# Performance work log

Measured on AMD Instinct MI355X. Metric: run time of the kernel, lower is better.

The kernel has to match this reference:

```python
import jax, jax.numpy as jnp
import numpy as np
from jax import lax

NPOINT = 2048
NSAMPLE = 32
RADIUS = 0.2


def setup_inputs() -> dict:
    key = jax.random.key(0)
    ks = jax.random.split(key, 6)
    B, N, C = 4, 16384, 64
    xyz = jax.random.normal(ks[0], (B, N, 3), jnp.float32)
    features = jax.random.normal(ks[1], (B, C, N), jnp.float32)

    def w(k, o, i):
        return jax.random.normal(k, (o, i), jnp.float32) * (1.0 / np.sqrt(i))

    W1 = w(ks[2], 64, C + 3)
    b1 = jnp.zeros((64,), jnp.float32)
    W2 = w(ks[3], 64, 64)
    b2 = jnp.zeros((64,), jnp.float32)
    W3 = w(ks[4], 128, 64)
    b3 = jnp.zeros((128,), jnp.float32)
    return {"xyz": xyz, "features": features, "W1": W1, "b1": b1,
            "W2": W2, "b2": b2, "W3": W3, "b3": b3}


def _fps(xyz, npoint):
    # Iterative furthest point sampling. xyz: (B, N, 3) -> (B, npoint) int32.
    B, N, _ = xyz.shape

    def step(carry, _):
        dist, last = carry  # dist: (B, N) running min sq-dist to chosen set
        p = jnp.take_along_axis(xyz, last[:, None, None], axis=1)  # (B,1,3)
        d = jnp.sum((xyz - p) ** 2, axis=-1)                        # (B,N)
        dist = jnp.minimum(dist, d)
        nxt = jnp.argmax(dist, axis=-1).astype(jnp.int32)
        return (dist, nxt), nxt

    init = (jnp.full((B, N), 1e10, xyz.dtype), jnp.zeros((B,), jnp.int32))
    _, rest = lax.scan(step, init, None, length=npoint - 1)  # (npoint-1, B)
    idx = jnp.concatenate([jnp.zeros((1, B), jnp.int32), rest], axis=0)
    return idx.T  # (B, npoint)


def _ball_query(xyz, new_xyz):
    # For each centroid pick up to NSAMPLE points within RADIUS (first-found
    # semantics, matching the PointNet++ CUDA ball_query: pad with first hit).
    B, N, _ = xyz.shape
    d2 = jnp.sum((new_xyz[:, :, None, :] - xyz[:, None, :, :]) ** 2, axis=-1)  # (B,S,N)
    cand = jnp.where(d2 < RADIUS * RADIUS, jnp.arange(N, dtype=jnp.int32), N)
    neg_vals, _ = lax.top_k(-cand, NSAMPLE)  # smallest NSAMPLE indices, in order
    sel = -neg_vals                           # (B,S,NSAMPLE)
    first = sel[..., :1]
    sel = jnp.where(sel == N, first, sel)     # pad empties with first hit
    return jnp.where(sel == N, 0, sel)        # fully-empty balls -> index 0


def reference(xyz, features, W1, b1, W2, b2, W3, b3):
    new_xyz_idx = _fps(xyz, NPOINT)                              # (B, S)
    new_xyz = jnp.take_along_axis(xyz, new_xyz_idx[..., None], axis=1)  # (B,S,3)
    idx = _ball_query(xyz, new_xyz)                              # (B,S,ns)
    B, S, ns = idx.shape
    C = features.shape[1]
    # Gather + center neighbor xyz: (B, 3, S, ns)
    gx = jnp.take_along_axis(xyz, idx.reshape(B, S * ns, 1), axis=1)
    gx = gx.reshape(B, S, ns, 3) - new_xyz[:, :, None, :]
    gx = gx.transpose(0, 3, 1, 2)
    # Gather neighbor features: (B, C, S, ns)
    gf = jnp.take_along_axis(features, idx.reshape(B, 1, S * ns), axis=2)
    gf = gf.reshape(B, C, S, ns)
    x = jnp.concatenate([gx, gf], axis=1)  # (B, C+3, S, ns)
    # SharedMLP: 1x1 conv + ReLU stack
    for W, b in ((W1, b1), (W2, b2), (W3, b3)):
        x = jax.nn.relu(jnp.einsum('oi,bisn->bosn', W, x) + b[None, :, None, None])
    new_features = x.max(axis=-1)  # (B, 128, S)
    return new_xyz, new_xyz_idx, new_features, idx
```

## Files before the change

kernel.cpp:

```cpp
#include <hip/hip_runtime.h>
#include <cstdint>

#define BATCH   4
#define NPTS    16384
#define NCH     64
#define NPOINT  2048
#define NSAMP   32

#define OFF_XYZ  0
#define OFF_IDX1 (BATCH*NPOINT*3)
#define OFF_FEAT (OFF_IDX1 + BATCH*NPOINT)
#define OFF_IDX3 (OFF_FEAT + BATCH*128*NPOINT)


__device__ __forceinline__ float sqd_exact(float dx, float dy, float dz) {
    float a = __fmul_rn(dx, dx);
    float b = __fmul_rn(dy, dy);
    float c = __fmul_rn(dz, dz);
    return __fadd_rn(__fadd_rn(a, b), c);
}

__device__ __forceinline__ int part3(int v) {
    return (v & 1) | ((v & 2) << 2) | ((v & 4) << 4) | ((v & 8) << 6);
}

__global__ __launch_bounds__(1024)
void binsort_kernel(const float* __restrict__ xyz, float* __restrict__ out) {
    const int b = blockIdx.x, t = threadIdx.x, lane = t & 63, wv = t >> 6;
    float* scr  = out + OFF_FEAT;
    float* sx   = scr + (size_t)b * NPTS;
    float* sy   = scr + (size_t)(BATCH + b) * NPTS;
    float* sz   = scr + (size_t)(2 * BATCH + b) * NPTS;
    int*   sidx = (int*)(scr + (size_t)3 * BATCH * NPTS) + (size_t)b * NPTS;
    const float* xb = xyz + (size_t)b * (NPTS * 3);

    __shared__ int hist[4096];
    __shared__ int wsum[16];
    for (int k = t; k < 4096; k += 1024) hist[k] = 0;
    __syncthreads();

    const int base = t << 4;
    float f[48];
    {
        const float4* v4 = (const float4*)(xb + (size_t)base * 3);
#pragma unroll
        for (int q = 0; q < 12; ++q) {
            float4 v = v4[q];
            f[4*q+0] = v.x; f[4*q+1] = v.y; f[4*q+2] = v.z; f[4*q+3] = v.w;
        }
    }
    int cells[16];
    const float sc = 16.0f / 9.0f;
#pragma unroll
    for (int j = 0; j < 16; ++j) {
        int qx = (int)fminf(fmaxf((f[3*j+0] + 4.5f) * sc, 0.0f), 15.0f);
        int qy = (int)fminf(fmaxf((f[3*j+1] + 4.5f) * sc, 0.0f), 15.0f);
        int qz = (int)fminf(fmaxf((f[3*j+2] + 4.5f) * sc, 0.0f), 15.0f);
        cells[j] = part3(qx) | (part3(qy) << 1) | (part3(qz) << 2);
        atomicAdd(&hist[cells[j]], 1);
    }
    __syncthreads();

    int h0 = hist[4*t], h1 = hist[4*t+1], h2 = hist[4*t+2], h3 = hist[4*t+3];
    int s = h0 + h1 + h2 + h3;
    int ps = s;
#pragma unroll
    for (int off = 1; off <= 32; off <<= 1) {
        int o = __shfl_up(ps, off, 64);
        if (lane >= off) ps += o;
    }
    if (lane == 63) wsum[wv] = ps;
    __syncthreads();
    int wbase = 0;
    for (int w = 0; w < wv; ++w) wbase += wsum[w];
    int excl = wbase + ps - s;
    hist[4*t]   = excl;
    hist[4*t+1] = excl + h0;
    hist[4*t+2] = excl + h0 + h1;
    hist[4*t+3] = excl + h0 + h1 + h2;
    __syncthreads();

#pragma unroll
    for (int j = 0; j < 16; ++j) {
        int pos = atomicAdd(&hist[cells[j]], 1);
        sx[pos] = f[3*j+0]; sy[pos] = f[3*j+1]; sz[pos] = f[3*j+2];
        sidx[pos] = base + j;
    }
}

__global__ __launch_bounds__(1024, 4)
void fps_kernel(const float* __restrict__ xyz, float* __restrict__ out) {
    const int b = blockIdx.x, t = threadIdx.x, lane = t & 63, wv = t >> 6;
    const float* scr  = out + OFF_FEAT;
    const float* sxp  = scr + (size_t)b * NPTS;
    const float* syp  = scr + (size_t)(BATCH + b) * NPTS;
    const float* szp  = scr + (size_t)(2 * BATCH + b) * NPTS;
    const int*   sip  = (const int*)(scr + (size_t)3 * BATCH * NPTS) + (size_t)b * NPTS;
    const float* __restrict__ xb = xyz + (size_t)b * (NPTS * 3);
    float* oxyz = out + OFF_XYZ  + (size_t)b * (NPOINT * 3);
    float* oidx = out + OFF_IDX1 + (size_t)b * NPOINT;

    const int base = t << 4;
    float px[16], py[16], pz[16], dist[16];
    unsigned idx2[8];
    {
        const float4* vx = (const float4*)(sxp + base);
        const float4* vy = (const float4*)(syp + base);
        const float4* vz = (const float4*)(szp + base);
        const int4*   vi = (const int4*)(sip + base);
#pragma unroll
        for (int q = 0; q < 4; ++q) {
            float4 a = vx[q]; px[4*q] = a.x; px[4*q+1] = a.y; px[4*q+2] = a.z; px[4*q+3] = a.w;
            float4 c = vy[q]; py[4*q] = c.x; py[4*q+1] = c.y; py[4*q+2] = c.z; py[4*q+3] = c.w;
            float4 d = vz[q]; pz[4*q] = d.x; pz[4*q+1] = d.y; pz[4*q+2] = d.z; pz[4*q+3] = d.w;
            int4   i = vi[q];
            idx2[2*q]   = (unsigned)i.x | ((unsigned)i.y << 16);
            idx2[2*q+1] = (unsigned)i.z | ((unsigned)i.w << 16);
        }
    }
    float bnx = px[0], bxx = px[0], bny = py[0], bxy = py[0], bnz = pz[0], bxz = pz[0];
#pragma unroll
    for (int j = 1; j < 16; ++j) {
        bnx = fminf(bnx, px[j]); bxx = fmaxf(bxx, px[j]);
        bny = fminf(bny, py[j]); bxy = fmaxf(bxy, py[j]);
        bnz = fminf(bnz, pz[j]); bxz = fmaxf(bxz, pz[j]);
    }
#pragma unroll
    for (int j = 0; j < 16; ++j) dist[j] = 1e10f;
    unsigned long long mk = 0;
    float maxdG = 1e10f;

    __shared__ unsigned long long s_k[2][16];

    float cx = xb[0], cy = xb[1], cz = xb[2];
    if (t == 0) { oxyz[0] = cx; oxyz[1] = cy; oxyz[2] = cz; oidx[0] = 0.0f; }

    for (int it = 1; it < NPOINT; ++it) {
        const int q = it & 1;
        float dxl = fmaxf(fmaxf(bnx - cx, cx - bxx), 0.0f);
        float dyl = fmaxf(fmaxf(bny - cy, cy - bxy), 0.0f);
        float dzl = fmaxf(fmaxf(bnz - cz, cz - bxz), 0.0f);
        float bb  = dxl * dxl + dyl * dyl + dzl * dzl;
        if (bb * 0.99999f < maxdG) {
            float mv = 0.0f;
#pragma unroll
            for (int j = 0; j < 16; ++j) {
                float d  = sqd_exact(__fsub_rn(px[j], cx),
                                     __fsub_rn(py[j], cy),
                                     __fsub_rn(pz[j], cz));
                float nd = fminf(dist[j], d);
                dist[j] = nd;
                mv = fmaxf(mv, nd);
            }
            int bi = 0xFFFF;
#pragma unroll
            for (int j = 0; j < 16; ++j) {
                int oi = (int)((idx2[j >> 1] >> ((j & 1) * 16)) & 0xFFFFu);
                if (dist[j] == mv) bi = min(bi, oi);
            }
            mk = ((unsigned long long)__float_as_uint(mv) << 32) | (unsigned)(~bi);
            maxdG = mv;
        }
        unsigned long long k = mk;
#pragma unroll
        for (int off = 32; off >= 1; off >>= 1) {
            unsigned long long o = __shfl_xor(k, off, 64);
            if (o > k) k = o;
        }
        if (lane == 0) s_k[q][wv] = k;
        __syncthreads();
        unsigned long long gk = s_k[q][0];
#pragma unroll
        for (int w = 1; w < 16; ++w) {
            unsigned long long v = s_k[q][w];
            if (v > gk) gk = v;
        }
        const int gi = (int)(~(unsigned)gk);
        cx = xb[gi*3+0]; cy = xb[gi*3+1]; cz = xb[gi*3+2];
        if (t == 0) {
            oxyz[it*3+0] = cx; oxyz[it*3+1] = cy; oxyz[it*3+2] = cz;
            oidx[it] = (float)gi;
        }
    }
}

__global__ __launch_bounds__(256)
void ballq_kernel(const float* __restrict__ xyz, float* __restrict__ out) {
    const int b    = blockIdx.y;
    const int t    = threadIdx.x;
    const int lane = t & 63;
    const int wv   = t >> 6;
    const int s    = blockIdx.x * 4 + wv;
    const float* __restrict__ xb = xyz + (size_t)b * (NPTS * 3);

    const float* ctr = out + OFF_XYZ + ((size_t)(b * NPOINT + s)) * 3;
    const float cx = ctr[0], cy = ctr[1], cz = ctr[2];

    __shared__ float sx[256], sy[256], sz[256];
    __shared__ int   lists[4][NSAMP];

    int have = 0;
    for (int tile = 0; tile < NPTS / 256; ++tile) {
        const int pi = tile * 256 + t;
        const float* p = xb + (size_t)pi * 3;
        float ax = p[0], ay = p[1], az = p[2];
        sx[t] = ax; sy[t] = ay; sz[t] = az;
        __syncthreads();
        if (have < NSAMP) {
#pragma unroll
            for (int sub = 0; sub < 4; ++sub) {
                const int li = sub * 64 + lane;
                float d2 = sqd_exact(__fsub_rn(cx, sx[li]),
                                     __fsub_rn(cy, sy[li]),
                                     __fsub_rn(cz, sz[li]));
                bool hit = d2 < 0.04f;
                unsigned long long m = __ballot(hit);
                if (hit) {
                    int pos = have + (int)__popcll(m & ((1ull << lane) - 1ull));
                    if (pos < NSAMP) lists[wv][pos] = tile * 256 + li;
                }
                have += (int)__popcll(m);
                if (have >= NSAMP) break;
            }
        }
        __syncthreads();
    }
    if (lane < NSAMP) {
        int hv = have < NSAMP ? have : NSAMP;
        int v0 = (have > 0) ? lists[wv][0] : 0;
        int v  = (lane < hv) ? lists[wv][lane] : v0;
        out[OFF_IDX3 + ((size_t)(b * NPOINT + s)) * NSAMP + lane] = (float)v;
    }
}

__global__ __launch_bounds__(256)
void mlp_kernel(const float* __restrict__ xyz, const float* __restrict__ feat,
                const float* __restrict__ W1, const float* __restrict__ b1,
                const float* __restrict__ W2, const float* __restrict__ b2,
                const float* __restrict__ W3, const float* __restrict__ b3,
                float* __restrict__ out) {
    const int s = blockIdx.x;
    const int b = blockIdx.y;
    const int t = threadIdx.x;

    __shared__ __align__(16) float Wbuf[64 * 128];
    __shared__ float Xs[67 * 32];
    __shared__ float H1[64 * 32];
    __shared__ float H2[64 * 32];
    __shared__ int   idxs[NSAMP];
    __shared__ float ctr[3];

    if (t < NSAMP) idxs[t] = (int)out[OFF_IDX3 + ((size_t)(b * NPOINT + s)) * NSAMP + t];
    if (t < 3)     ctr[t]  = out[OFF_XYZ + ((size_t)(b * NPOINT + s)) * 3 + t];
    for (int k = t; k < 67 * 64; k += 256) {
        int i = k >> 6, o = k & 63;
        Wbuf[k] = W1[o * 67 + i];
    }
    __syncthreads();

    const float* xb = xyz  + (size_t)b * (NPTS * 3);
    const float* fb = feat + (size_t)b * (NCH * NPTS);
    for (int k = t; k < 67 * 32; k += 256) {
        int i = k >> 5, n = k & 31;
        int ii = idxs[n];
        float v;
        if (i < 3) v = __fsub_rn(xb[(size_t)ii * 3 + i], ctr[i]);
        else       v = fb[(size_t)(i - 3) * NPTS + ii];
        Xs[k] = v;
    }
    __syncthreads();

    const int n  = t & 31;
    const int og = t >> 5;

    {
        const int o0 = og * 8;
        float acc[8] = {0,0,0,0,0,0,0,0};
        for (int i = 0; i < 67; ++i) {
            float x = Xs[i * 32 + n];
            const float4* wp = (const float4*)&Wbuf[i * 64 + o0];
            float4 w0 = wp[0], w1 = wp[1];
            acc[0] += w0.x * x; acc[1] += w0.y * x; acc[2] += w0.z * x; acc[3] += w0.w * x;
            acc[4] += w1.x * x; acc[5] += w1.y * x; acc[6] += w1.z * x; acc[7] += w1.w * x;
        }
#pragma unroll
        for (int k = 0; k < 8; ++k)
            H1[(o0 + k) * 32 + n] = fmaxf(acc[k] + b1[o0 + k], 0.0f);
    }
    __syncthreads();
    for (int k = t; k < 64 * 64; k += 256) {
        int i = k >> 6, o = k & 63;
        Wbuf[k] = W2[o * 64 + i];
    }
    __syncthreads();

    {
        const int o0 = og * 8;
        float acc[8] = {0,0,0,0,0,0,0,0};
        for (int i = 0; i < 64; ++i) {
            float x = H1[i * 32 + n];
            const float4* wp = (const float4*)&Wbuf[i * 64 + o0];
            float4 w0 = wp[0], w1 = wp[1];
            acc[0] += w0.x * x; acc[1] += w0.y * x; acc[2] += w0.z * x; acc[3] += w0.w * x;
            acc[4] += w1.x * x; acc[5] += w1.y * x; acc[6] += w1.z * x; acc[7] += w1.w * x;
        }
#pragma unroll
        for (int k = 0; k < 8; ++k)
            H2[(o0 + k) * 32 + n] = fmaxf(acc[k] + b2[o0 + k], 0.0f);
    }
    __syncthreads();
    for (int k = t; k < 64 * 128; k += 256) {
        int i = k >> 7, o = k & 127;
        Wbuf[k] = W3[o * 64 + i];
    }
    __syncthreads();

    {
        const int o0 = og * 16;
        float acc[16];
#pragma unroll
        for (int k = 0; k < 16; ++k) acc[k] = 0.0f;
        for (int i = 0; i < 64; ++i) {
            float x = H2[i * 32 + n];
            const float4* wp = (const float4*)&Wbuf[i * 128 + o0];
            float4 w0 = wp[0], w1 = wp[1], w2 = wp[2], w3 = wp[3];
            acc[0]  += w0.x * x; acc[1]  += w0.y * x; acc[2]  += w0.z * x; acc[3]  += w0.w * x;
            acc[4]  += w1.x * x; acc[5]  += w1.y * x; acc[6]  += w1.z * x; acc[7]  += w1.w * x;
            acc[8]  += w2.x * x; acc[9]  += w2.y * x; acc[10] += w2.z * x; acc[11] += w2.w * x;
            acc[12] += w3.x * x; acc[13] += w3.y * x; acc[14] += w3.z * x; acc[15] += w3.w * x;
        }
#pragma unroll
        for (int k = 0; k < 16; ++k) {
            float h = fmaxf(acc[k] + b3[o0 + k], 0.0f);
#pragma unroll
            for (int off = 16; off >= 1; off >>= 1)
                h = fmaxf(h, __shfl_xor(h, off, 64));
            if (n == 0)
                out[OFF_FEAT + (size_t)b * 128 * NPOINT + (size_t)(o0 + k) * NPOINT + s] = h;
        }
    }
}

extern "C" void kernel_launch(void* const* d_in, const int* in_sizes, int n_in,
                              void* d_out, int out_size, void* d_ws, size_t ws_size,
                              hipStream_t stream) {
    const float* xyz  = (const float*)d_in[0];
    const float* feat = (const float*)d_in[1];
    const float* W1   = (const float*)d_in[2];
    const float* b1   = (const float*)d_in[3];
    const float* W2   = (const float*)d_in[4];
    const float* b2   = (const float*)d_in[5];
    const float* W3   = (const float*)d_in[6];
    const float* b3   = (const float*)d_in[7];
    float* out = (float*)d_out;

    binsort_kernel<<<BATCH, 1024, 0, stream>>>(xyz, out);
    fps_kernel<<<BATCH, 1024, 0, stream>>>(xyz, out);
    ballq_kernel<<<dim3(NPOINT / 4, BATCH), 256, 0, stream>>>(xyz, out);
    mlp_kernel<<<dim3(NPOINT, BATCH), 256, 0, stream>>>(xyz, feat, W1, b1, W2, b2, W3, b3, out);
}
```

Baseline: 3.336 ms.

## Restructure FPS argmax reduction to carry winner coordinates and avoid global reload

The FPS loop now tracks the argmax index and its coordinates inside each thread's update, replacing the packed 64-bit key with a float max shuffle plus ballot-based tie-breaking. The cross-wave reduction is done by 16 threads with shuffles, and the winner's coordinates are broadcast through shared memory. This removes the dependent global load of the next centroid and the serial 16-way scan on every thread. The cost is a second __syncthreads per iteration and extra select work per point.

After: 6.333 ms. 89.9% more time.

```diff
diff --git a/kernel.cpp b/kernel.cpp
--- a/kernel.cpp
+++ b/kernel.cpp
@@ -90,7 +90,7 @@
 
 __global__ __launch_bounds__(1024, 4)
 void fps_kernel(const float* __restrict__ xyz, float* __restrict__ out) {
-    const int b = blockIdx.x, t = threadIdx.x, lane = t & 63, wv = t >> 6;
+    const int b = blockIdx.x, t = threadIdx.x, wv = t >> 6;
     const float* scr  = out + OFF_FEAT;
     const float* sxp  = scr + (size_t)b * NPTS;
     const float* syp  = scr + (size_t)(BATCH + b) * NPTS;
@@ -127,22 +127,26 @@
     }
 #pragma unroll
     for (int j = 0; j < 16; ++j) dist[j] = 1e10f;
-    unsigned long long mk = 0;
-    float maxdG = 1e10f;
-
-    __shared__ unsigned long long s_k[2][16];
+
+    float mv = 1e30f;
+    int   bi = 0x7FFFFFFF;
+    float wx = px[0], wy = py[0], wz = pz[0];
+
+    __shared__ float2 s_meta[16];
+    __shared__ __align__(16) float4 s_coord[16];
+    __shared__ __align__(16) float4 s_final;
 
     float cx = xb[0], cy = xb[1], cz = xb[2];
     if (t == 0) { oxyz[0] = cx; oxyz[1] = cy; oxyz[2] = cz; oidx[0] = 0.0f; }
 
     for (int it = 1; it < NPOINT; ++it) {
-        const int q = it & 1;
         float dxl = fmaxf(fmaxf(bnx - cx, cx - bxx), 0.0f);
         float dyl = fmaxf(fmaxf(bny - cy, cy - bxy), 0.0f);
         float dzl = fmaxf(fmaxf(bnz - cz, cz - bxz), 0.0f);
         float bb  = dxl * dxl + dyl * dyl + dzl * dzl;
-        if (bb * 0.99999f < maxdG) {
-            float mv = 0.0f;
+        if (bb * 0.99999f < mv) {
+            float nmv = -1.0f; int nbi = 0x7FFFFFFF;
+            float nwx = px[0], nwy = py[0], nwz = pz[0];
 #pragma unroll
             for (int j = 0; j < 16; ++j) {
                 float d  = sqd_exact(__fsub_rn(px[j], cx),
@@ -150,36 +154,60 @@
                                      __fsub_rn(pz[j], cz));
                 float nd = fminf(dist[j], d);
                 dist[j] = nd;
-                mv = fmaxf(mv, nd);
+                int oi = (int)((idx2[j >> 1] >> ((j & 1) * 16)) & 0xFFFFu);
+                bool better = (nd > nmv) || ((nd == nmv) & (oi < nbi));
+                nmv = better ? nd : nmv;
+                nbi = better ? oi : nbi;
+                nwx = better ? px[j] : nwx;
+                nwy = better ? py[j] : nwy;
+                nwz = better ? pz[j] : nwz;
             }
-            int bi = 0xFFFF;
-#pragma unroll
-            for (int j = 0; j < 16; ++j) {
-                int oi = (int)((idx2[j >> 1] >> ((j & 1) * 16)) & 0xFFFFu);
-                if (dist[j] == mv) bi = min(bi, oi);
+            mv = nmv; bi = nbi; wx = nwx; wy = nwy; wz = nwz;
+        }
+        float wm = mv;
+#pragma unroll
+        for (int off = 32; off >= 1; off >>= 1)
+            wm = fmaxf(wm, __shfl_xor(wm, off, 64));
+        bool cand = (mv == wm);
+        unsigned long long msk = __ballot(cand);
+        if (__popcll(msk) > 1) {
+            int tb = 0x7FFFFFFF;
+            unsigned long long m2 = msk;
+            while (m2) {
+                int l = __ffsll(m2) - 1;
+                int obi = __shfl(bi, l, 64);
+                tb = min(tb, obi);
+                m2 &= m2 - 1;
             }
-            mk = ((unsigned long long)__float_as_uint(mv) << 32) | (unsigned)(~bi);
-            maxdG = mv;
-        }
-        unsigned long long k = mk;
-#pragma unroll
-        for (int off = 32; off >= 1; off >>= 1) {
-            unsigned long long o = __shfl_xor(k, off, 64);
-            if (o > k) k = o;
-        }
-        if (lane == 0) s_k[q][wv] = k;
+            cand = cand && (bi == tb);
+        }
+        if (cand) {
+            s_meta[wv]  = make_float2(wm, __int_as_float(bi));
+            s_coord[wv] = make_float4(wx, wy, wz, __int_as_float(bi));
+        }
         __syncthreads();
-        unsigned long long gk = s_k[q][0];
-#pragma unroll
-        for (int w = 1; w < 16; ++w) {
-            unsigned long long v = s_k[q][w];
-            if (v > gk) gk = v;
-        }
-        const int gi = (int)(~(unsigned)gk);
-        cx = xb[gi*3+0]; cy = xb[gi*3+1]; cz = xb[gi*3+2];
+        if (t < 16) {
+            float2 me = s_meta[t];
+            float4 mc = s_coord[t];
+            float v  = me.x;
+            int   vb = __float_as_int(me.y);
+#pragma unroll
+            for (int off = 1; off <= 8; off <<= 1) {
+                float v2  = __shfl_xor(v, off, 16);
+                int   vb2 = __shfl_xor(vb, off, 16);
+                bool take = (v2 > v) || ((v2 == v) & (vb2 < vb));
+                v  = take ? v2 : v;
+                vb = take ? vb2 : vb;
+            }
+            if (__float_as_int(me.y) == vb)
+                s_final = mc;
+        }
+        __syncthreads();
+        float4 f = s_final;
+        cx = f.x; cy = f.y; cz = f.z;
         if (t == 0) {
             oxyz[it*3+0] = cx; oxyz[it*3+1] = cy; oxyz[it*3+2] = cz;
-            oidx[it] = (float)gi;
+            oidx[it] = (float)__float_as_int(f.w);
         }
     }
 }
```
